# Performance work log

Hardware: AMD Instinct MI355X
Metric: run time of the kernel (lower is better)

The kernel has to match this reference:

```python
import jax, jax.numpy as jnp
import numpy as np

N = 100000


def seg_mean(feat, src, dst, n):
    # gather at src, scatter-mean at dst (PyG mean aggr: 0 for isolated nodes)
    s = jax.ops.segment_sum(feat[src], dst, num_segments=n)
    cnt = jax.ops.segment_sum(jnp.ones((src.shape[0],), feat.dtype), dst, num_segments=n)
    return s / jnp.maximum(cnt, 1.0)[:, None]


def setup_inputs() -> dict:
    key = jax.random.key(0)
    ks = jax.random.split(key, 8)
    d_in, d_h = 64, 32
    E = 1_250_000
    inp = {
        "x": jax.random.normal(ks[0], (N, d_in), jnp.float32),
        "W1_pos": jax.random.normal(ks[1], (2 * d_in, d_h), jnp.float32) * 0.05,
        "b1_pos": jnp.zeros((d_h,), jnp.float32),
        "W1_neg": jax.random.normal(ks[2], (2 * d_in, d_h), jnp.float32) * 0.05,
        "b1_neg": jnp.zeros((d_h,), jnp.float32),
        "W2_pos": jax.random.normal(ks[3], (3 * d_h, d_h), jnp.float32) * 0.05,
        "b2_pos": jnp.zeros((d_h,), jnp.float32),
        "W2_neg": jax.random.normal(ks[4], (3 * d_h, d_h), jnp.float32) * 0.05,
        "b2_neg": jnp.zeros((d_h,), jnp.float32),
        "pos_edge_index": jax.random.randint(ks[5], (2, E), 0, N, jnp.int64),
        "neg_edge_index": jax.random.randint(ks[6], (2, E), 0, N, jnp.int64),
    }
    return inp


def reference(x, W1_pos, b1_pos, W1_neg, b1_neg, W2_pos, b2_pos, W2_neg, b2_neg,
              pos_edge_index, neg_edge_index):
    ps, pd = pos_edge_index[0], pos_edge_index[1]
    ns, nd = neg_edge_index[0], neg_edge_index[1]
    n = x.shape[0]

    # --- layer 1 (first_aggr=True) ---
    ap = seg_mean(x, ps, pd, n)          # [N, 64]
    an = seg_mean(x, ns, nd, n)
    out_p = jnp.concatenate([ap, x], -1) @ W1_pos + b1_pos   # [N, 32]
    out_n = jnp.concatenate([an, x], -1) @ W1_neg + b1_neg
    z = jnp.tanh(jnp.concatenate([out_p, out_n], -1))        # [N, 64]

    # --- layer 2 (first_aggr=False) ---
    d_h = out_p.shape[-1]
    zp, zn = z[:, :d_h], z[:, d_h:]
    out_p = jnp.concatenate([seg_mean(zp, ps, pd, n), seg_mean(zn, ns, nd, n), zp], -1) @ W2_pos + b2_pos
    out_n = jnp.concatenate([seg_mean(zn, ps, pd, n), seg_mean(zp, ns, nd, n), zn], -1) @ W2_neg + b2_neg
    z = jnp.tanh(jnp.concatenate([out_p, out_n], -1))
    return z
```

## Files before the change

kernel.cpp:

```cpp
#include <hip/hip_runtime.h>
#include <math.h>


typedef _Float16 h2 __attribute__((ext_vector_type(2)));
typedef _Float16 h4 __attribute__((ext_vector_type(4)));

__device__ inline float fdot2f(h2 a, h2 b, float c) {
#if __has_builtin(__builtin_amdgcn_fdot2)
    return __builtin_amdgcn_fdot2(a, b, c, false);
#else
    return fmaf((float)a.x, (float)b.x, fmaf((float)a.y, (float)b.y, c));
#endif
}

__device__ inline h4 shflx4(h4 v, int m) {
    int2 i = __builtin_bit_cast(int2, v);
    i.x = __shfl_xor(i.x, m);
    i.y = __shfl_xor(i.y, m);
    return __builtin_bit_cast(h4, i);
}

__device__ inline float fast_tanh(float v) {
    float e = __expf(2.0f * v);
    return 1.0f - 2.0f / (e + 1.0f);
}


#define BSHIFT 9
#define BSIZE  512
#define NBMAX  512
#define CAP    8192

__global__ void __launch_bounds__(256) bucket_k(
    const int* __restrict__ pos, const int* __restrict__ neg,
    int* __restrict__ pcnt, unsigned* __restrict__ ebuf,
    int E, int n, int nb)
{
    __shared__ int cnt[NBMAX], gbase[NBMAX], lcnt[NBMAX];
    const int K = 16;
    int tid = threadIdx.x;
    int base = blockIdx.x * (256 * K);

    for (int i = tid; i < nb; i += 256) cnt[i] = 0;
    __syncthreads();

    unsigned val[K];
    int part[K];
    #pragma unroll
    for (int k = 0; k < K; ++k) {
        int e = base + k * 256 + tid;
        part[k] = -1;
        if (e < 2 * E) {
            int nd, sr;
            if (e < E) { nd = pos[E + e];                 sr = pos[e]; }
            else       { int ee = e - E; nd = n + neg[E + ee]; sr = neg[ee]; }
            int p = nd >> BSHIFT;
            part[k] = p;
            val[k] = ((unsigned)(nd & (BSIZE - 1)) << 17) | (unsigned)sr;
            atomicAdd(&cnt[p], 1);
        }
    }
    __syncthreads();
    for (int i = tid; i < nb; i += 256) {
        int c = cnt[i];
        gbase[i] = c ? atomicAdd(&pcnt[i], c) : 0;
        lcnt[i] = 0;
    }
    __syncthreads();
    #pragma unroll
    for (int k = 0; k < K; ++k) {
        int p = part[k];
        if (p >= 0) {
            int off = gbase[p] + atomicAdd(&lcnt[p], 1);
            if (off < CAP) ebuf[(size_t)p * CAP + off] = val[k];
        }
    }
}

__global__ void __launch_bounds__(512) bscan_k(
    const int* __restrict__ pcnt, int* __restrict__ bbase, int nb)
{
    __shared__ int s[512];
    int tid = threadIdx.x;
    int v = (tid < nb) ? pcnt[tid] : 0;
    s[tid] = v;
    __syncthreads();
    for (int off = 1; off < 512; off <<= 1) {
        int t = (tid >= off) ? s[tid - off] : 0;
        __syncthreads();
        s[tid] += t;
        __syncthreads();
    }
    if (tid < nb) bbase[tid] = s[tid] - v;
}

__global__ void __launch_bounds__(256) scatter_k(
    const unsigned* __restrict__ ebuf, const int* __restrict__ pcnt,
    const int* __restrict__ bbase,
    int* __restrict__ cur, int* __restrict__ col, int n)
{
    __shared__ int lcnt[BSIZE], lbase[BSIZE], sc[256];
    __shared__ int lcol[CAP];
    int p = blockIdx.x;
    int tid = threadIdx.x;
    int n2 = 2 * n;
    int lo = p << BSHIFT;
    int nn = min(BSIZE, n2 - lo);
    int cnt = min(pcnt[p], CAP);
    const unsigned* buf = ebuf + (size_t)p * CAP;

    lcnt[tid] = 0; lcnt[tid + 256] = 0;
    __syncthreads();
    for (int i = tid; i < cnt; i += 256) {
        unsigned v = buf[i];
        atomicAdd(&lcnt[v >> 17], 1);
    }
    __syncthreads();
    int a0 = lcnt[2 * tid], a1 = lcnt[2 * tid + 1];
    int s = a0 + a1;
    sc[tid] = s;
    __syncthreads();
    for (int off = 1; off < 256; off <<= 1) {
        int t = (tid >= off) ? sc[tid - off] : 0;
        __syncthreads();
        sc[tid] += t;
        __syncthreads();
    }
    int excl = sc[tid] - s;
    lbase[2 * tid] = excl;
    lbase[2 * tid + 1] = excl + a0;
    __syncthreads();
    int gb = bbase[p];
    for (int i = tid; i < nn; i += 256)
        cur[lo + i] = gb + lbase[i] + lcnt[i];
    __syncthreads();
    for (int i = tid; i < cnt; i += 256) {
        unsigned v = buf[i];
        int rel = (int)(v >> 17);
        int slot = atomicAdd(&lbase[rel], 1);
        lcol[slot] = (int)(v & 0x1FFFFu);
    }
    __syncthreads();
    for (int t = tid; t < cnt; t += 256)
        col[gb + t] = lcol[t];
}


__global__ void __launch_bounds__(256) cvt_k(
    const float4* __restrict__ x, h4* __restrict__ xh, int n4)
{
    int i = blockIdx.x * 256 + threadIdx.x;
    if (i < n4) {
        float4 v = x[i];
        h4 o = { (_Float16)v.x, (_Float16)v.y, (_Float16)v.z, (_Float16)v.w };
        xh[i] = o;
    }
}


__global__ void __launch_bounds__(256, 8) layer1_pull(
    const h4* __restrict__ xh,
    const int* __restrict__ cur, const int* __restrict__ col,
    const float* __restrict__ W1p, const float* __restrict__ b1p,
    const float* __restrict__ W1n, const float* __restrict__ b1n,
    _Float16* __restrict__ zh, int n)
{
    __shared__ h4 Wq[32 * 64];
    __shared__ h4 vec4s[4][48];
    int tid = threadIdx.x;
    for (int idx = tid; idx < 32 * 64; idx += 256) {
        int j4 = idx >> 6, c = idx & 63, cw = c & 31;
        const float* Ws = (c < 32) ? W1p : W1n;
        int r = 4 * j4;
        Wq[idx] = h4{ (_Float16)Ws[r * 32 + cw],       (_Float16)Ws[(r + 1) * 32 + cw],
                      (_Float16)Ws[(r + 2) * 32 + cw], (_Float16)Ws[(r + 3) * 32 + cw] };
    }
    __syncthreads();

    int wave = tid >> 6, lane = tid & 63;
    int g = lane >> 4, f = lane & 15;
    int c = lane;
    float bb = (c < 32) ? b1p[c] : b1n[c - 32];
    int ab4 = (c < 32) ? 0 : 16;
    h4* vec = vec4s[wave];

    int stride = gridDim.x * 4;
    for (int node = blockIdx.x * 4 + wave; node < n; node += stride) {
        int p0 = node ? cur[node - 1] : 0;
        int p1 = cur[node];
        int q0 = cur[n + node - 1];
        int q1 = cur[n + node];

        h4 a = {}, b = {};
        #pragma unroll 2
        for (int it = p0 + g; it < p1; it += 4) {
            h4 t = xh[(unsigned)(col[it] * 16 + f)];
            a = a + t;
        }
        #pragma unroll 2
        for (int it = q0 + g; it < q1; it += 4) {
            h4 t = xh[(unsigned)(col[it] * 16 + f)];
            b = b + t;
        }
        a = a + shflx4(a, 16); a = a + shflx4(a, 32);
        b = b + shflx4(b, 16); b = b + shflx4(b, 32);
        _Float16 rp = (_Float16)(1.0f / (float)max(p1 - p0, 1));
        _Float16 rq = (_Float16)(1.0f / (float)max(q1 - q0, 1));
        h4 rpv = { rp, rp, rp, rp }, rqv = { rq, rq, rq, rq };
        a = a * rpv;
        b = b * rqv;
        h4 xi = xh[(unsigned)(node * 16 + f)];
        h4 sv = (g == 0) ? a : (g == 1) ? b : xi;
        if (g < 3) vec[g * 16 + f] = sv;
        __builtin_amdgcn_wave_barrier();

        float acc = bb;
        #pragma unroll
        for (int j4 = 0; j4 < 16; ++j4) {
            h4 v = vec[ab4 + j4];
            h4 w = Wq[j4 * 64 + c];
            h2 vl = { v.x, v.y }, vh = { v.z, v.w };
            h2 wl = { w.x, w.y }, wh = { w.z, w.w };
            acc = fdot2f(vl, wl, acc);
            acc = fdot2f(vh, wh, acc);
        }
        #pragma unroll
        for (int j4 = 0; j4 < 16; ++j4) {
            h4 v = vec[32 + j4];
            h4 w = Wq[(16 + j4) * 64 + c];
            h2 vl = { v.x, v.y }, vh = { v.z, v.w };
            h2 wl = { w.x, w.y }, wh = { w.z, w.w };
            acc = fdot2f(vl, wl, acc);
            acc = fdot2f(vh, wh, acc);
        }
        zh[(unsigned)(node * 64 + c)] = (_Float16)fast_tanh(acc);
        __builtin_amdgcn_wave_barrier();
    }
}

__global__ void __launch_bounds__(256, 8) layer2_pull(
    const h4* __restrict__ zh4,
    const int* __restrict__ cur, const int* __restrict__ col,
    const float* __restrict__ W2p, const float* __restrict__ b2p,
    const float* __restrict__ W2n, const float* __restrict__ b2n,
    float* __restrict__ out, int n)
{
    __shared__ h4 Wq[24 * 64];
    __shared__ h4 vec4s[4][48];
    int tid = threadIdx.x;
    for (int idx = tid; idx < 24 * 64; idx += 256) {
        int j4 = idx >> 6, c = idx & 63, cw = c & 31;
        const float* Ws = (c < 32) ? W2p : W2n;
        int r = 4 * j4;
        Wq[idx] = h4{ (_Float16)Ws[r * 32 + cw],       (_Float16)Ws[(r + 1) * 32 + cw],
                      (_Float16)Ws[(r + 2) * 32 + cw], (_Float16)Ws[(r + 3) * 32 + cw] };
    }
    __syncthreads();

    int wave = tid >> 6, lane = tid & 63;
    int g = lane >> 4, f = lane & 15;
    int c = lane;
    float bb = (c < 32) ? b2p[c] : b2n[c - 32];
    int s1 = (c < 32) ? 0 : 8;
    int s2 = (c < 32) ? 24 : 16;
    int s3 = (c < 32) ? 32 : 40;
    h4* vec = vec4s[wave];

    int stride = gridDim.x * 4;
    for (int node = blockIdx.x * 4 + wave; node < n; node += stride) {
        int p0 = node ? cur[node - 1] : 0;
        int p1 = cur[node];
        int q0 = cur[n + node - 1];
        int q1 = cur[n + node];

        h4 a = {}, b = {};
        #pragma unroll 2
        for (int it = p0 + g; it < p1; it += 4) {
            h4 t = zh4[(unsigned)(col[it] * 16 + f)];
            a = a + t;
        }
        #pragma unroll 2
        for (int it = q0 + g; it < q1; it += 4) {
            h4 t = zh4[(unsigned)(col[it] * 16 + f)];
            b = b + t;
        }
        a = a + shflx4(a, 16); a = a + shflx4(a, 32);
        b = b + shflx4(b, 16); b = b + shflx4(b, 32);
        _Float16 rp = (_Float16)(1.0f / (float)max(p1 - p0, 1));
        _Float16 rq = (_Float16)(1.0f / (float)max(q1 - q0, 1));
        h4 rpv = { rp, rp, rp, rp }, rqv = { rq, rq, rq, rq };
        a = a * rpv;
        b = b * rqv;
        h4 zi = zh4[(unsigned)(node * 16 + f)];
        h4 sv = (g == 0) ? a : (g == 1) ? b : zi;
        if (g < 3) vec[g * 16 + f] = sv;
        __builtin_amdgcn_wave_barrier();

        float acc = bb;
        #pragma unroll
        for (int j4 = 0; j4 < 8; ++j4) {
            h4 v = vec[s1 + j4];
            h4 w = Wq[j4 * 64 + c];
            h2 vl = { v.x, v.y }, vh = { v.z, v.w };
            h2 wl = { w.x, w.y }, wh = { w.z, w.w };
            acc = fdot2f(vl, wl, acc);
            acc = fdot2f(vh, wh, acc);
        }
        #pragma unroll
        for (int j4 = 0; j4 < 8; ++j4) {
            h4 v = vec[s2 + j4];
            h4 w = Wq[(8 + j4) * 64 + c];
            h2 vl = { v.x, v.y }, vh = { v.z, v.w };
            h2 wl = { w.x, w.y }, wh = { w.z, w.w };
            acc = fdot2f(vl, wl, acc);
            acc = fdot2f(vh, wh, acc);
        }
        #pragma unroll
        for (int j4 = 0; j4 < 8; ++j4) {
            h4 v = vec[s3 + j4];
            h4 w = Wq[(16 + j4) * 64 + c];
            h2 vl = { v.x, v.y }, vh = { v.z, v.w };
            h2 wl = { w.x, w.y }, wh = { w.z, w.w };
            acc = fdot2f(vl, wl, acc);
            acc = fdot2f(vh, wh, acc);
        }
        out[(size_t)node * 64 + c] = fast_tanh(acc);
        __builtin_amdgcn_wave_barrier();
    }
}

extern "C" void kernel_launch(void* const* d_in, const int* in_sizes, int n_in,
                              void* d_out, int out_size, void* d_ws, size_t ws_size,
                              hipStream_t stream)
{
    const float* x   = (const float*)d_in[0];
    const float* W1p = (const float*)d_in[1];
    const float* b1p = (const float*)d_in[2];
    const float* W1n = (const float*)d_in[3];
    const float* b1n = (const float*)d_in[4];
    const float* W2p = (const float*)d_in[5];
    const float* b2p = (const float*)d_in[6];
    const float* W2n = (const float*)d_in[7];
    const float* b2n = (const float*)d_in[8];
    const int*   pos = (const int*)d_in[9];
    const int*   neg = (const int*)d_in[10];

    int n = in_sizes[0] / 64;
    int E = in_sizes[9] / 2;
    int n2 = 2 * n;
    int nb = (n2 + BSIZE - 1) / BSIZE;

    int*      pcnt  = (int*)d_ws;
    int*      bbase = pcnt + NBMAX;
    int*      cur   = bbase + NBMAX;
    int*      col   = cur + n2;
    unsigned* ebuf  = (unsigned*)(col + 2 * (size_t)E);
    _Float16* zh    = (_Float16*)ebuf;
    _Float16* xh    = zh + (size_t)n * 64;

    hipMemsetAsync(pcnt, 0, NBMAX * sizeof(int), stream);

    int bblocks = (2 * E + 4095) / 4096;
    bucket_k<<<bblocks, 256, 0, stream>>>(pos, neg, pcnt, ebuf, E, n, nb);
    bscan_k <<<1, 512, 0, stream>>>(pcnt, bbase, nb);
    scatter_k<<<nb, 256, 0, stream>>>(ebuf, pcnt, bbase, cur, col, n);

    int n4 = n * 16;
    cvt_k  <<<(n4 + 255) / 256, 256, 0, stream>>>((const float4*)x, (h4*)xh, n4);

    int lblocks = 2048;
    layer1_pull<<<lblocks, 256, 0, stream>>>((const h4*)xh, cur, col,
                                             W1p, b1p, W1n, b1n, zh, n);
    layer2_pull<<<lblocks, 256, 0, stream>>>((const h4*)zh, cur, col,
                                             W2p, b2p, W2n, b2n,
                                             (float*)d_out, n);
}
```

Before: 286.7 us.

## Split fused pull layers into aggregation and MFMA GEMM kernels

Each layer's fused gather-plus-fdot2 kernel is replaced by two kernels. A gather/mean kernel writes the aggregated features to a scratch buffer held in the output array, and a GEMM kernel multiplies [agg, self] tiles by pre-packed fp16 weights using 16x16x32 MFMA instructions, then applies bias and tanh. A prep kernel packs both weight matrices once per call into the MFMA B-fragment layout, with zero padding for the block structure. Bucketing also reuses the rank returned by the first shared atomic, which removes a second atomic pass. The split adds an extra round trip of the aggregated features through global memory and two more launches per call.

After: 300.0 us. 1.05x slower.

```diff
diff --git a/kernel.cpp b/kernel.cpp
--- a/kernel.cpp
+++ b/kernel.cpp
@@ -2,16 +2,9 @@
 #include <math.h>
 
 
-typedef _Float16 h2 __attribute__((ext_vector_type(2)));
 typedef _Float16 h4 __attribute__((ext_vector_type(4)));
-
-__device__ inline float fdot2f(h2 a, h2 b, float c) {
-#if __has_builtin(__builtin_amdgcn_fdot2)
-    return __builtin_amdgcn_fdot2(a, b, c, false);
-#else
-    return fmaf((float)a.x, (float)b.x, fmaf((float)a.y, (float)b.y, c));
-#endif
-}
+typedef _Float16 h8 __attribute__((ext_vector_type(8)));
+typedef float f32x4 __attribute__((ext_vector_type(4)));
 
 __device__ inline h4 shflx4(h4 v, int m) {
     int2 i = __builtin_bit_cast(int2, v);
@@ -36,7 +29,7 @@
     int* __restrict__ pcnt, unsigned* __restrict__ ebuf,
     int E, int n, int nb)
 {
-    __shared__ int cnt[NBMAX], gbase[NBMAX], lcnt[NBMAX];
+    __shared__ int cnt[NBMAX], gbase[NBMAX];
     const int K = 16;
     int tid = threadIdx.x;
     int base = blockIdx.x * (256 * K);
@@ -45,7 +38,7 @@
     __syncthreads();
 
     unsigned val[K];
-    int part[K];
+    int part[K], rank[K];
     #pragma unroll
     for (int k = 0; k < K; ++k) {
         int e = base + k * 256 + tid;
@@ -57,21 +50,20 @@
             int p = nd >> BSHIFT;
             part[k] = p;
             val[k] = ((unsigned)(nd & (BSIZE - 1)) << 17) | (unsigned)sr;
-            atomicAdd(&cnt[p], 1);
+            rank[k] = atomicAdd(&cnt[p], 1);
         }
     }
     __syncthreads();
     for (int i = tid; i < nb; i += 256) {
         int c = cnt[i];
         gbase[i] = c ? atomicAdd(&pcnt[i], c) : 0;
-        lcnt[i] = 0;
     }
     __syncthreads();
     #pragma unroll
     for (int k = 0; k < K; ++k) {
         int p = part[k];
         if (p >= 0) {
-            int off = gbase[p] + atomicAdd(&lcnt[p], 1);
+            int off = gbase[p] + rank[k];
             if (off < CAP) ebuf[(size_t)p * CAP + off] = val[k];
         }
     }
@@ -158,174 +150,139 @@
 }
 
 
-__global__ void __launch_bounds__(256, 8) layer1_pull(
-    const h4* __restrict__ xh,
+__device__ inline float b1map(const float* W1p, const float* W1n, int k, int c)
+{
+    if (c < 32) {
+        if (k < 64)   return W1p[k * 32 + c];
+        if (k >= 128) return W1p[(k - 64) * 32 + c];
+        return 0.0f;
+    } else {
+        int cn = c - 32;
+        if (k >= 64)  return W1n[(k - 64) * 32 + cn];
+        return 0.0f;
+    }
+}
+
+__device__ inline float b2map(const float* W2p, const float* W2n, int k, int c)
+{
+    if (c < 32) {
+        if (k < 32)               return W2p[k * 32 + c];
+        if (k >= 96 && k < 128)   return W2p[(k - 96 + 32) * 32 + c];
+        if (k >= 128 && k < 160)  return W2p[(k - 128 + 64) * 32 + c];
+        return 0.0f;
+    } else {
+        int cn = c - 32;
+        if (k >= 32 && k < 64)    return W2n[(k - 32) * 32 + cn];
+        if (k >= 64 && k < 96)    return W2n[(k - 64 + 32) * 32 + cn];
+        if (k >= 160)             return W2n[(k - 160 + 64) * 32 + cn];
+        return 0.0f;
+    }
+}
+
+__global__ void __launch_bounds__(256) prep_k(
+    const float* __restrict__ W1p, const float* __restrict__ W1n,
+    const float* __restrict__ W2p, const float* __restrict__ W2n,
+    _Float16* __restrict__ Bpack)
+{
+    int slot = blockIdx.x * 256 + threadIdx.x;
+    if (slot >= 2 * 24 * 64) return;
+    int mat  = slot / (24 * 64);
+    int rem  = slot % (24 * 64);
+    int fg   = rem / 64;
+    int lane = rem % 64;
+    int kk = fg >> 2, nt = fg & 3;
+    int g = lane >> 4, m = lane & 15;
+    _Float16* dst = Bpack + (size_t)slot * 8;
+    int c = nt * 16 + m;
+    #pragma unroll
+    for (int j = 0; j < 8; ++j) {
+        int k = kk * 32 + g * 8 + j;
+        float v = mat ? b2map(W2p, W2n, k, c) : b1map(W1p, W1n, k, c);
+        dst[j] = (_Float16)v;
+    }
+}
+
+
+__global__ void __launch_bounds__(256) agg_k(
+    const h4* __restrict__ feat4,
     const int* __restrict__ cur, const int* __restrict__ col,
-    const float* __restrict__ W1p, const float* __restrict__ b1p,
-    const float* __restrict__ W1n, const float* __restrict__ b1n,
-    _Float16* __restrict__ zh, int n)
-{
-    __shared__ h4 Wq[32 * 64];
-    __shared__ h4 vec4s[4][48];
-    int tid = threadIdx.x;
-    for (int idx = tid; idx < 32 * 64; idx += 256) {
-        int j4 = idx >> 6, c = idx & 63, cw = c & 31;
-        const float* Ws = (c < 32) ? W1p : W1n;
-        int r = 4 * j4;
-        Wq[idx] = h4{ (_Float16)Ws[r * 32 + cw],       (_Float16)Ws[(r + 1) * 32 + cw],
-                      (_Float16)Ws[(r + 2) * 32 + cw], (_Float16)Ws[(r + 3) * 32 + cw] };
-    }
-    __syncthreads();
-
+    h4* __restrict__ ag4, int n)
+{
+    int tid = threadIdx.x;
     int wave = tid >> 6, lane = tid & 63;
     int g = lane >> 4, f = lane & 15;
-    int c = lane;
-    float bb = (c < 32) ? b1p[c] : b1n[c - 32];
-    int ab4 = (c < 32) ? 0 : 16;
-    h4* vec = vec4s[wave];
+    int list = g >> 1;
+    int sub = g & 1;
 
     int stride = gridDim.x * 4;
     for (int node = blockIdx.x * 4 + wave; node < n; node += stride) {
-        int p0 = node ? cur[node - 1] : 0;
-        int p1 = cur[node];
-        int q0 = cur[n + node - 1];
-        int q1 = cur[n + node];
-
-        h4 a = {}, b = {};
+        int idx = list ? n + node : node;
+        int r0 = idx ? cur[idx - 1] : 0;
+        int r1 = cur[idx];
+
+        h4 acc = { (_Float16)0, (_Float16)0, (_Float16)0, (_Float16)0 };
         #pragma unroll 2
-        for (int it = p0 + g; it < p1; it += 4) {
-            h4 t = xh[(unsigned)(col[it] * 16 + f)];
-            a = a + t;
+        for (int it = r0 + sub; it < r1; it += 2)
+            acc = acc + feat4[(unsigned)(col[it] * 16 + f)];
+        acc = acc + shflx4(acc, 16);
+        _Float16 inv = (_Float16)(1.0f / (float)max(r1 - r0, 1));
+        h4 iv = { inv, inv, inv, inv };
+        acc = acc * iv;
+        if (sub == 0)
+            ag4[(unsigned)(node * 32 + list * 16 + f)] = acc;
+    }
+}
+
+
+#define ROWP 200
+
+__global__ void __launch_bounds__(256) gemm_k(
+    const h4* __restrict__ ag4, const h4* __restrict__ feat4,
+    const h8* __restrict__ Bp,
+    const float* __restrict__ bp, const float* __restrict__ bn,
+    float* __restrict__ outf, _Float16* __restrict__ outh,
+    int f32out, int n)
+{
+    __shared__ _Float16 A_lds[64 * ROWP];
+    int tid = threadIdx.x;
+    int base = blockIdx.x * 64;
+
+    for (int ch = tid; ch < 64 * 24; ch += 256) {
+        int r = ch / 24, p = ch % 24;
+        int row = min(base + r, n - 1);
+        h8 v = (p < 16) ? ((const h8*)ag4)[(size_t)row * 16 + p]
+                        : ((const h8*)feat4)[(size_t)row * 8 + (p - 16)];
+        *(h8*)&A_lds[r * ROWP + p * 8] = v;
+    }
+    __syncthreads();
+
+    int w = tid >> 6, lane = tid & 63;
+    int m = lane & 15, g = lane >> 4;
+
+    h8 a[6];
+    #pragma unroll
+    for (int kk = 0; kk < 6; ++kk)
+        a[kk] = *(const h8*)&A_lds[(w * 16 + m) * ROWP + kk * 32 + g * 8];
+
+    #pragma unroll
+    for (int nt = 0; nt < 4; ++nt) {
+        f32x4 acc = { 0.f, 0.f, 0.f, 0.f };
+        #pragma unroll
+        for (int kk = 0; kk < 6; ++kk) {
+            h8 b = Bp[(kk * 4 + nt) * 64 + lane];
+            acc = __builtin_amdgcn_mfma_f32_16x16x32_f16(a[kk], b, acc, 0, 0, 0);
         }
-        #pragma unroll 2
-        for (int it = q0 + g; it < q1; it += 4) {
-            h4 t = xh[(unsigned)(col[it] * 16 + f)];
-            b = b + t;
+        int colc = nt * 16 + m;
+        float bias = (colc < 32) ? bp[colc] : bn[colc - 32];
+        #pragma unroll
+        for (int reg = 0; reg < 4; ++reg) {
+            int node = base + w * 16 + g * 4 + reg;
+            if (node < n) {
+                float val = fast_tanh(acc[reg] + bias);
+                if (f32out) outf[(size_t)node * 64 + colc] = val;
+                else        outh[(size_t)node * 64 + colc] = (_Float16)val;
+            }
         }
-        a = a + shflx4(a, 16); a = a + shflx4(a, 32);
-        b = b + shflx4(b, 16); b = b + shflx4(b, 32);
-        _Float16 rp = (_Float16)(1.0f / (float)max(p1 - p0, 1));
-        _Float16 rq = (_Float16)(1.0f / (float)max(q1 - q0, 1));
-        h4 rpv = { rp, rp, rp, rp }, rqv = { rq, rq, rq, rq };
-        a = a * rpv;
-        b = b * rqv;
-        h4 xi = xh[(unsigned)(node * 16 + f)];
-        h4 sv = (g == 0) ? a : (g == 1) ? b : xi;
-        if (g < 3) vec[g * 16 + f] = sv;
-        __builtin_amdgcn_wave_barrier();
-
-        float acc = bb;
-        #pragma unroll
-        for (int j4 = 0; j4 < 16; ++j4) {
-            h4 v = vec[ab4 + j4];
-            h4 w = Wq[j4 * 64 + c];
-            h2 vl = { v.x, v.y }, vh = { v.z, v.w };
-            h2 wl = { w.x, w.y }, wh = { w.z, w.w };
-            acc = fdot2f(vl, wl, acc);
-            acc = fdot2f(vh, wh, acc);
-        }
-        #pragma unroll
-        for (int j4 = 0; j4 < 16; ++j4) {
-            h4 v = vec[32 + j4];
-            h4 w = Wq[(16 + j4) * 64 + c];
-            h2 vl = { v.x, v.y }, vh = { v.z, v.w };
-            h2 wl = { w.x, w.y }, wh = { w.z, w.w };
-            acc = fdot2f(vl, wl, acc);
-            acc = fdot2f(vh, wh, acc);
-        }
-        zh[(unsigned)(node * 64 + c)] = (_Float16)fast_tanh(acc);
-        __builtin_amdgcn_wave_barrier();
-    }
-}
-
-__global__ void __launch_bounds__(256, 8) layer2_pull(
-    const h4* __restrict__ zh4,
-    const int* __restrict__ cur, const int* __restrict__ col,
-    const float* __restrict__ W2p, const float* __restrict__ b2p,
-    const float* __restrict__ W2n, const float* __restrict__ b2n,
-    float* __restrict__ out, int n)
-{
-    __shared__ h4 Wq[24 * 64];
-    __shared__ h4 vec4s[4][48];
-    int tid = threadIdx.x;
-    for (int idx = tid; idx < 24 * 64; idx += 256) {
-        int j4 = idx >> 6, c = idx & 63, cw = c & 31;
-        const float* Ws = (c < 32) ? W2p : W2n;
-        int r = 4 * j4;
-        Wq[idx] = h4{ (_Float16)Ws[r * 32 + cw],       (_Float16)Ws[(r + 1) * 32 + cw],
-                      (_Float16)Ws[(r + 2) * 32 + cw], (_Float16)Ws[(r + 3) * 32 + cw] };
-    }
-    __syncthreads();
-
-    int wave = tid >> 6, lane = tid & 63;
-    int g = lane >> 4, f = lane & 15;
-    int c = lane;
-    float bb = (c < 32) ? b2p[c] : b2n[c - 32];
-    int s1 = (c < 32) ? 0 : 8;
-    int s2 = (c < 32) ? 24 : 16;
-    int s3 = (c < 32) ? 32 : 40;
-    h4* vec = vec4s[wave];
-
-    int stride = gridDim.x * 4;
-    for (int node = blockIdx.x * 4 + wave; node < n; node += stride) {
-        int p0 = node ? cur[node - 1] : 0;
-        int p1 = cur[node];
-        int q0 = cur[n + node - 1];
-        int q1 = cur[n + node];
-
-        h4 a = {}, b = {};
-        #pragma unroll 2
-        for (int it = p0 + g; it < p1; it += 4) {
-            h4 t = zh4[(unsigned)(col[it] * 16 + f)];
-            a = a + t;
-        }
-        #pragma unroll 2
-        for (int it = q0 + g; it < q1; it += 4) {
-            h4 t = zh4[(unsigned)(col[it] * 16 + f)];
-            b = b + t;
-        }
-        a = a + shflx4(a, 16); a = a + shflx4(a, 32);
-        b = b + shflx4(b, 16); b = b + shflx4(b, 32);
-        _Float16 rp = (_Float16)(1.0f / (float)max(p1 - p0, 1));
-        _Float16 rq = (_Float16)(1.0f / (float)max(q1 - q0, 1));
-        h4 rpv = { rp, rp, rp, rp }, rqv = { rq, rq, rq, rq };
-        a = a * rpv;
-        b = b * rqv;
-        h4 zi = zh4[(unsigned)(node * 16 + f)];
-        h4 sv = (g == 0) ? a : (g == 1) ? b : zi;
-        if (g < 3) vec[g * 16 + f] = sv;
-        __builtin_amdgcn_wave_barrier();
-
-        float acc = bb;
-        #pragma unroll
-        for (int j4 = 0; j4 < 8; ++j4) {
-            h4 v = vec[s1 + j4];
-            h4 w = Wq[j4 * 64 + c];
-            h2 vl = { v.x, v.y }, vh = { v.z, v.w };
-            h2 wl = { w.x, w.y }, wh = { w.z, w.w };
-            acc = fdot2f(vl, wl, acc);
-            acc = fdot2f(vh, wh, acc);
-        }
-        #pragma unroll
-        for (int j4 = 0; j4 < 8; ++j4) {
-            h4 v = vec[s2 + j4];
-            h4 w = Wq[(8 + j4) * 64 + c];
-            h2 vl = { v.x, v.y }, vh = { v.z, v.w };
-            h2 wl = { w.x, w.y }, wh = { w.z, w.w };
-            acc = fdot2f(vl, wl, acc);
-            acc = fdot2f(vh, wh, acc);
-        }
-        #pragma unroll
-        for (int j4 = 0; j4 < 8; ++j4) {
-            h4 v = vec[s3 + j4];
-            h4 w = Wq[(16 + j4) * 64 + c];
-            h2 vl = { v.x, v.y }, vh = { v.z, v.w };
-            h2 wl = { w.x, w.y }, wh = { w.z, w.w };
-            acc = fdot2f(vl, wl, acc);
-            acc = fdot2f(vh, wh, acc);
-        }
-        out[(size_t)node * 64 + c] = fast_tanh(acc);
-        __builtin_amdgcn_wave_barrier();
     }
 }
 
@@ -354,9 +311,11 @@
     int*      bbase = pcnt + NBMAX;
     int*      cur   = bbase + NBMAX;
     int*      col   = cur + n2;
-    unsigned* ebuf  = (unsigned*)(col + 2 * (size_t)E);
+    _Float16* Bpack = (_Float16*)(col + 2 * (size_t)E);
+    _Float16* xh    = Bpack + 2 * 24 * 64 * 8;
+    unsigned* ebuf  = (unsigned*)(xh + (size_t)n * 64);
     _Float16* zh    = (_Float16*)ebuf;
-    _Float16* xh    = zh + (size_t)n * 64;
+    h4*       ag4   = (h4*)d_out;
 
     hipMemsetAsync(pcnt, 0, NBMAX * sizeof(int), stream);
 
@@ -366,12 +325,18 @@
     scatter_k<<<nb, 256, 0, stream>>>(ebuf, pcnt, bbase, cur, col, n);
 
     int n4 = n * 16;
-    cvt_k  <<<(n4 + 255) / 256, 256, 0, stream>>>((const float4*)x, (h4*)xh, n4);
-
-    int lblocks = 2048;
-    layer1_pull<<<lblocks, 256, 0, stream>>>((const h4*)xh, cur, col,
-                                             W1p, b1p, W1n, b1n, zh, n);
-    layer2_pull<<<lblocks, 256, 0, stream>>>((const h4*)zh, cur, col,
-                                             W2p, b2p, W2n, b2n,
-                                             (float*)d_out, n);
-}
+    cvt_k <<<(n4 + 255) / 256, 256, 0, stream>>>((const float4*)x, (h4*)xh, n4);
+    prep_k<<<12, 256, 0, stream>>>(W1p, W1n, W2p, W2n, Bpack);
+
+    int ablocks = 2048;
+    int gblocks = (n + 63) / 64;
+
+    agg_k <<<ablocks, 256, 0, stream>>>((const h4*)xh, cur, col, ag4, n);
+    gemm_k<<<gblocks, 256, 0, stream>>>(ag4, (const h4*)xh, (const h8*)Bpack,
+                                        b1p, b1n, nullptr, zh, 0, n);
+
+    agg_k <<<ablocks, 256, 0, stream>>>((const h4*)zh, cur, col, ag4, n);
+    gemm_k<<<gblocks, 256, 0, stream>>>(ag4, (const h4*)zh,
+                                        (const h8*)(Bpack + 24 * 64 * 8),
+                                        b2p, b2n, (float*)d_out, nullptr, 1, n);
+}
```
